# Kernel tuning notes

Hardware: AMD Instinct MI355X
Metric: run time of the kernel (lower is better)

## Reference

```python
import jax, jax.numpy as jnp
import numpy as np

NUM_USERS = 50000
NUM_ITEMS = 20000
N_NODES = NUM_USERS + NUM_ITEMS
D = 128
CONTENT_DIM = 512
BATCH = 8192
N_EDGES = 500000
NEG_SLOPE = 0.2  # GATConv leaky_relu slope


def setup_inputs() -> dict:
    key = jax.random.key(0)
    ks = jax.random.split(key, 16)
    return {
        "user_ids": jax.random.randint(ks[0], (BATCH,), 0, NUM_USERS),
        "item_ids": jax.random.randint(ks[1], (BATCH,), 0, NUM_ITEMS),
        "content_features": jax.random.normal(ks[2], (BATCH, CONTENT_DIM), jnp.float32),
        "edge_index": jax.random.randint(ks[3], (2, N_EDGES), 0, N_NODES),
        "user_emb_w": jax.random.normal(ks[4], (NUM_USERS, D), jnp.float32) * 0.05,
        "item_emb_w": jax.random.normal(ks[5], (NUM_ITEMS, D), jnp.float32) * 0.05,
        "content_proj_w": jax.random.normal(ks[6], (D, CONTENT_DIM), jnp.float32) * 0.04,
        "content_proj_b": jnp.zeros((D,), jnp.float32),
        "conv1_lin_w": jax.random.normal(ks[7], (2 * D, 2 * D), jnp.float32) * 0.06,
        "conv1_att_src": jax.random.normal(ks[8], (2, D), jnp.float32) * 0.1,
        "conv1_att_dst": jax.random.normal(ks[9], (2, D), jnp.float32) * 0.1,
        "conv1_bias": jnp.zeros((2 * D,), jnp.float32),
        "conv2_lin_w": jax.random.normal(ks[10], (D, 2 * D), jnp.float32) * 0.06,
        "conv2_att_src": jax.random.normal(ks[11], (1, D), jnp.float32) * 0.1,
        "conv2_att_dst": jax.random.normal(ks[12], (1, D), jnp.float32) * 0.1,
        "conv2_bias": jnp.zeros((D,), jnp.float32),
        "pred_w1": jax.random.normal(ks[13], (D, 3 * D), jnp.float32) * 0.05,
        "pred_b1": jnp.zeros((D,), jnp.float32),
        "pred_w2": jax.random.normal(ks[14], (1, D), jnp.float32) * 0.09,
        "pred_b2": jnp.zeros((1,), jnp.float32),
    }


def gat_conv(x, src, dst, lin_w, att_src, att_dst, bias, heads, out_ch):
    # PyG GATConv (shared lin for src/dst, concat=True, add_self_loops handled outside)
    n = x.shape[0]
    h = (x @ lin_w.T).reshape(n, heads, out_ch)          # [N,H,C]
    a_src = jnp.sum(h * att_src, axis=-1)                # [N,H]
    a_dst = jnp.sum(h * att_dst, axis=-1)                # [N,H]
    alpha = jax.nn.leaky_relu(a_src[src] + a_dst[dst], NEG_SLOPE)  # [E,H]
    # softmax over incoming edges of each destination node
    amax = jax.ops.segment_max(alpha, dst, num_segments=n)
    ex = jnp.exp(alpha - amax[dst])
    denom = jax.ops.segment_sum(ex, dst, num_segments=n)
    w = ex / denom[dst]                                  # [E,H]
    out = jax.ops.segment_sum(h[src] * w[:, :, None], dst, num_segments=n)
    return out.reshape(n, heads * out_ch) + bias


def _forward(user_ids, item_ids, edge_index, content_features, user_emb_w, item_emb_w,
             content_proj_w, content_proj_b, conv1_lin_w, conv1_att_src, conv1_att_dst,
             conv1_bias, conv2_lin_w, conv2_att_src, conv2_att_dst, conv2_bias,
             pred_w1, pred_b1, pred_w2, pred_b2):
    u_emb = user_emb_w[user_ids]                         # [B,D]
    i_emb = item_emb_w[item_ids]                         # [B,D]
    c_emb = content_features @ content_proj_w.T + content_proj_b  # [B,D]
    # scatter-init sparse node features (only batch nodes are nonzero, as in source)
    x = jnp.zeros((N_NODES, 2 * D), jnp.float32)
    x = x.at[user_ids].set(jnp.concatenate([u_emb, jnp.zeros_like(c_emb)], axis=1))
    x = x.at[NUM_USERS + item_ids].set(jnp.concatenate([i_emb, c_emb], axis=1))
    # add self loops (fill_value irrelevant: edge_weight unused by GATConv)
    loops = jnp.arange(N_NODES, dtype=edge_index.dtype)
    src = jnp.concatenate([edge_index[0], loops])
    dst = jnp.concatenate([edge_index[1], loops])
    x = jax.nn.elu(gat_conv(x, src, dst, conv1_lin_w, conv1_att_src, conv1_att_dst, conv1_bias, 2, D))
    # dropout inactive (eval mode)
    x = gat_conv(x, src, dst, conv2_lin_w, conv2_att_src, conv2_att_dst, conv2_bias, 1, D)
    combined = jnp.concatenate([u_emb, x[NUM_USERS + item_ids], x[user_ids]], axis=1)  # [B,3D]
    h = jax.nn.relu(combined @ pred_w1.T + pred_b1)
    return (h @ pred_w2.T + pred_b2).squeeze(-1)         # [B]


def reference(user_ids, item_ids, content_features, edge_index, user_emb_w, item_emb_w,
              content_proj_w, content_proj_b, conv1_lin_w, conv1_att_src, conv1_att_dst,
              conv1_bias, conv2_lin_w, conv2_att_src, conv2_att_dst, conv2_bias,
              pred_w1, pred_b1, pred_w2, pred_b2):
    return _forward(user_ids, item_ids, edge_index, content_features, user_emb_w, item_emb_w,
                    content_proj_w, content_proj_b, conv1_lin_w, conv1_att_src, conv1_att_dst,
                    conv1_bias, conv2_lin_w, conv2_att_src, conv2_att_dst, conv2_bias,
                    pred_w1, pred_b1, pred_w2, pred_b2)
```

## Files before the change

kernel.cpp:

```cpp
#include <hip/hip_runtime.h>
#include <hip/hip_bf16.h>

#define NU 50000
#define NI 20000
#define NN 70000
#define DD 128
#define BB 8192
#define EE 500000
#define ET 570000
#define NTASK 16384

__device__ __forceinline__ float lrelu(float x) { return x > 0.f ? x : 0.2f * x; }

typedef __attribute__((ext_vector_type(8))) short bf16x8;
typedef __attribute__((ext_vector_type(8))) unsigned short u16x8;
typedef __attribute__((ext_vector_type(4))) float f32x4;

__device__ __forceinline__ unsigned short f2bf_rne(float f) {
  unsigned int u = __builtin_bit_cast(unsigned int, f);
  u += 0x7FFFu + ((u >> 16) & 1u);
  return (unsigned short)(u >> 16);
}
__device__ __forceinline__ float bf2f(unsigned short h) {
  unsigned int u = ((unsigned int)h) << 16;
  return __builtin_bit_cast(float, u);
}

__global__ void split4_kernel(const float* __restrict__ w0, unsigned short* h0, unsigned short* l0, int n0,
                              const float* __restrict__ w1, unsigned short* h1, unsigned short* l1, int n1,
                              const float* __restrict__ w2, unsigned short* h2, unsigned short* l2, int n2,
                              const float* __restrict__ w3, unsigned short* h3, unsigned short* l3, int n3) {
  int i = blockIdx.x * 256 + threadIdx.x;
  const float* w; unsigned short* h; unsigned short* l; int idx;
  if (i < n0) { w = w0; h = h0; l = l0; idx = i; }
  else if (i < n0 + n1) { w = w1; h = h1; l = l1; idx = i - n0; }
  else if (i < n0 + n1 + n2) { w = w2; h = h2; l = l2; idx = i - n0 - n1; }
  else if (i < n0 + n1 + n2 + n3) { w = w3; h = h3; l = l3; idx = i - n0 - n1 - n2; }
  else return;
  float f = w[idx];
  unsigned short hh = f2bf_rne(f);
  h[idx] = hh;
  l[idx] = (unsigned short)(__builtin_bit_cast(unsigned int, f - bf2f(hh)) >> 16);
}

template <int GATHER>
__global__ __launch_bounds__(256) void gemm_mfma(
    const float* __restrict__ A,
    const unsigned short* __restrict__ Bh, const unsigned short* __restrict__ Bl,
    const float* __restrict__ bias, float* __restrict__ C,
    int M, int N, int K, int act,
    const int* __restrict__ uidx, const float* __restrict__ gA0,
    const float* __restrict__ gA1) {
  __shared__ __align__(16) unsigned short sAh[8][64][8];
  __shared__ __align__(16) unsigned short sAl[8][64][8];
  __shared__ __align__(16) unsigned short sBh[8][64][8];
  __shared__ __align__(16) unsigned short sBl[8][64][8];
  int tid = threadIdx.x;
  int bm = blockIdx.x * 64, bn = blockIdx.y * 64;
  int lane = tid & 63, w = tid >> 6;
  int wr = (w >> 1) * 32, wc = (w & 1) * 32;
  int fr = lane & 15, fk = lane >> 4;
  f32x4 acc[2][2] = {};

  for (int k0 = 0; k0 < K; k0 += 64) {
    __syncthreads();
#pragma unroll
    for (int t = 0; t < 2; t++) {
      int f = tid + t * 256;
      int row = f >> 3, kb = f & 7;
      int kg = k0 + kb * 8;
      const float* ap;
      if (GATHER) {
        int sec = kg >> 7;
        int kc = kg & 127;
        int r = bm + row;
        if (sec == 0)      ap = &gA0[(size_t)uidx[r] * 128 + kc];
        else if (sec == 1) ap = &gA1[((size_t)(BB + r)) * 128 + kc];
        else               ap = &gA1[((size_t)r) * 128 + kc];
      } else {
        ap = &A[(size_t)(bm + row) * K + kg];
      }
      float4 v0 = *reinterpret_cast<const float4*>(ap);
      float4 v1 = *reinterpret_cast<const float4*>(ap + 4);
      float vv[8] = {v0.x, v0.y, v0.z, v0.w, v1.x, v1.y, v1.z, v1.w};
      u16x8 hv, lv;
#pragma unroll
      for (int j = 0; j < 8; j++) {
        unsigned short hh = f2bf_rne(vv[j]);
        hv[j] = hh;
        lv[j] = (unsigned short)(__builtin_bit_cast(unsigned int, vv[j] - bf2f(hh)) >> 16);
      }
      *reinterpret_cast<u16x8*>(&sAh[kb][row][0]) = hv;
      *reinterpret_cast<u16x8*>(&sAl[kb][row][0]) = lv;
    }
#pragma unroll
    for (int t = 0; t < 2; t++) {
      int f = tid + t * 256;
      int row = f >> 3, kb = f & 7;
      int kg = k0 + kb * 8;
      *reinterpret_cast<u16x8*>(&sBh[kb][row][0]) =
          *reinterpret_cast<const u16x8*>(&Bh[(size_t)(bn + row) * K + kg]);
      *reinterpret_cast<u16x8*>(&sBl[kb][row][0]) =
          *reinterpret_cast<const u16x8*>(&Bl[(size_t)(bn + row) * K + kg]);
    }
    __syncthreads();
#pragma unroll
    for (int s = 0; s < 2; s++) {
      int kb = s * 4 + fk;
      bf16x8 ah0 = *reinterpret_cast<const bf16x8*>(&sAh[kb][wr + fr][0]);
      bf16x8 ah1 = *reinterpret_cast<const bf16x8*>(&sAh[kb][wr + 16 + fr][0]);
      bf16x8 al0 = *reinterpret_cast<const bf16x8*>(&sAl[kb][wr + fr][0]);
      bf16x8 al1 = *reinterpret_cast<const bf16x8*>(&sAl[kb][wr + 16 + fr][0]);
      bf16x8 bh0 = *reinterpret_cast<const bf16x8*>(&sBh[kb][wc + fr][0]);
      bf16x8 bh1 = *reinterpret_cast<const bf16x8*>(&sBh[kb][wc + 16 + fr][0]);
      bf16x8 bl0 = *reinterpret_cast<const bf16x8*>(&sBl[kb][wc + fr][0]);
      bf16x8 bl1 = *reinterpret_cast<const bf16x8*>(&sBl[kb][wc + 16 + fr][0]);
      acc[0][0] = __builtin_amdgcn_mfma_f32_16x16x32_bf16(al0, bh0, acc[0][0], 0, 0, 0);
      acc[0][0] = __builtin_amdgcn_mfma_f32_16x16x32_bf16(ah0, bl0, acc[0][0], 0, 0, 0);
      acc[0][0] = __builtin_amdgcn_mfma_f32_16x16x32_bf16(ah0, bh0, acc[0][0], 0, 0, 0);
      acc[0][1] = __builtin_amdgcn_mfma_f32_16x16x32_bf16(al0, bh1, acc[0][1], 0, 0, 0);
      acc[0][1] = __builtin_amdgcn_mfma_f32_16x16x32_bf16(ah0, bl1, acc[0][1], 0, 0, 0);
      acc[0][1] = __builtin_amdgcn_mfma_f32_16x16x32_bf16(ah0, bh1, acc[0][1], 0, 0, 0);
      acc[1][0] = __builtin_amdgcn_mfma_f32_16x16x32_bf16(al1, bh0, acc[1][0], 0, 0, 0);
      acc[1][0] = __builtin_amdgcn_mfma_f32_16x16x32_bf16(ah1, bl0, acc[1][0], 0, 0, 0);
      acc[1][0] = __builtin_amdgcn_mfma_f32_16x16x32_bf16(ah1, bh0, acc[1][0], 0, 0, 0);
      acc[1][1] = __builtin_amdgcn_mfma_f32_16x16x32_bf16(al1, bh1, acc[1][1], 0, 0, 0);
      acc[1][1] = __builtin_amdgcn_mfma_f32_16x16x32_bf16(ah1, bl1, acc[1][1], 0, 0, 0);
      acc[1][1] = __builtin_amdgcn_mfma_f32_16x16x32_bf16(ah1, bh1, acc[1][1], 0, 0, 0);
    }
  }
#pragma unroll
  for (int j = 0; j < 2; j++) {
    int col = bn + wc + j * 16 + fr;
    float bj = bias ? bias[col] : 0.f;
#pragma unroll
    for (int i = 0; i < 2; i++) {
#pragma unroll
      for (int r = 0; r < 4; r++) {
        int row = bm + wr + i * 16 + fk * 4 + r;
        float v = acc[i][j][r] + bj;
        if (act == 1) v = fmaxf(v, 0.f);
        C[(size_t)row * N + col] = v;
      }
    }
  }
}

__global__ void deg_winner_kernel(const int* __restrict__ ei, const int* __restrict__ iid,
                                  int* __restrict__ deg, int* __restrict__ winner) {
  int e = blockIdx.x * 256 + threadIdx.x;
  if (e < BB) atomicMax(&winner[iid[e]], e);
  if (e >= ET) return;
  int dst = (e < EE) ? ei[EE + e] : (e - EE);
  atomicAdd(&deg[dst], 1);
}

__global__ void build_xa_kernel(const int* __restrict__ uid, const int* __restrict__ iid,
                                const int* __restrict__ winner,
                                const float* __restrict__ uemb, const float* __restrict__ iemb,
                                const float* __restrict__ cemb,
                                float* __restrict__ Xa, int* __restrict__ map) {
  int t = blockIdx.x;
  int lane = threadIdx.x;
  int c4 = lane * 4;
  float4 v = make_float4(0.f, 0.f, 0.f, 0.f);
  int node;
  if (t < BB) {
    int u = uid[t];
    node = u;
    if (c4 < DD) v = *reinterpret_cast<const float4*>(&uemb[(size_t)u * DD + c4]);
  } else {
    int b = t - BB;
    int it = iid[b];
    node = NU + it;
    if (c4 < DD) {
      v = *reinterpret_cast<const float4*>(&iemb[(size_t)it * DD + c4]);
    } else {
      int wb = winner[it];
      v = *reinterpret_cast<const float4*>(&cemb[(size_t)wb * DD + (c4 - DD)]);
    }
  }
  *reinterpret_cast<float4*>(&Xa[(size_t)t * 256 + c4]) = v;
  if (lane == 0) map[node] = t;
}

__global__ void mark_kernel(const int* __restrict__ ei, const int* __restrict__ map,
                            unsigned char* __restrict__ needed) {
  int e = blockIdx.x * 256 + threadIdx.x;
  if (e >= ET) return;
  int src, dst;
  if (e < EE) { src = ei[e]; dst = ei[EE + e]; }
  else { src = e - EE; dst = src; }
  if (map[dst] >= 0) needed[src] = 1;
}

__global__ void rowstart_kernel(const int* __restrict__ deg, int* __restrict__ rowstart,
                                int* __restrict__ fill, int* __restrict__ counter) {
  int v = blockIdx.x * 256 + threadIdx.x;
  if (v >= NN) return;
  int s = atomicAdd(counter, deg[v]);
  rowstart[v] = s;
  fill[v] = s;
}

__global__ void fill_kernel(const int* __restrict__ ei, int* __restrict__ fill,
                            int* __restrict__ col) {
  int e = blockIdx.x * 256 + threadIdx.x;
  if (e >= ET) return;
  int src, dst;
  if (e < EE) { src = ei[e]; dst = ei[EE + e]; }
  else { src = e - EE; dst = src; }
  int pos = atomicAdd(&fill[dst], 1);
  col[pos] = src;
}

__global__ __launch_bounds__(256) void a1q_kernel(
    const int* __restrict__ uid, const int* __restrict__ iid,
    const float* __restrict__ Ha,
    const float* __restrict__ atts, const float* __restrict__ attd,
    const float* __restrict__ w2,
    const float* __restrict__ att2s, const float* __restrict__ att2d,
    float* __restrict__ a1s, float* __restrict__ a1d,
    float* __restrict__ qs, float* __restrict__ qd) {
  int t = blockIdx.x * 4 + (threadIdx.x >> 6);
  int lane = threadIdx.x & 63;
  if (t >= NTASK) {
    int k = (t - NTASK) * 64 + lane;
    float s = 0.f, d = 0.f;
#pragma unroll 4
    for (int j = 0; j < DD; j++) {
      float w = w2[(size_t)j * 256 + k];
      s += att2s[j] * w;
      d += att2d[j] * w;
    }
    qs[k] = s;
    qd[k] = d;
    return;
  }
  int v = (t < BB) ? uid[t] : NU + iid[t - BB];
  int head = lane >> 5, c = (lane & 31) * 4;
  float4 hv = *reinterpret_cast<const float4*>(&Ha[(size_t)t * 256 + head * DD + c]);
  float4 sv = *reinterpret_cast<const float4*>(&atts[head * DD + c]);
  float4 dv = *reinterpret_cast<const float4*>(&attd[head * DD + c]);
  float ps = hv.x * sv.x + hv.y * sv.y + hv.z * sv.z + hv.w * sv.w;
  float pd = hv.x * dv.x + hv.y * dv.y + hv.z * dv.z + hv.w * dv.w;
  for (int o = 1; o < 32; o <<= 1) { ps += __shfl_xor(ps, o); pd += __shfl_xor(pd, o); }
  if ((lane & 31) == 0) {
    a1s[(size_t)v * 2 + head] = ps;
    a1d[(size_t)v * 2 + head] = pd;
  }
}

__global__ __launch_bounds__(256) void conv1_agg_kernel(
    const int* __restrict__ col, const int* __restrict__ rowstart,
    const int* __restrict__ deg, const float* __restrict__ Ha,
    const int* __restrict__ map, const unsigned char* __restrict__ needed,
    const float* __restrict__ a1s, const float* __restrict__ a1d,
    const float* __restrict__ bias,
    const float* __restrict__ qs, const float* __restrict__ qd,
    unsigned short* __restrict__ x1b, float* __restrict__ a2s, float* __restrict__ a2d) {
  int v = blockIdx.x * 4 + (threadIdx.x >> 6);
  int lane = threadIdx.x & 63;
  if (!needed[v]) return;
  int head = lane >> 5;
  int d = deg[v], s0 = rowstart[v];
  float2 adv = *reinterpret_cast<const float2*>(&a1d[(size_t)v * 2]);
  float4 acc = make_float4(0.f, 0.f, 0.f, 0.f);
  float den;
  if (d <= 64) {
    bool act = lane < d;
    int ci = act ? col[s0 + lane] : 0;
    float2 asv = make_float2(0.f, 0.f);
    int ri = -1;
    if (act) {
      asv = *reinterpret_cast<const float2*>(&a1s[(size_t)ci * 2]);
      ri = map[ci];
    }
    float al0 = act ? lrelu(asv.x + adv.x) : -1e30f;
    float al1 = act ? lrelu(asv.y + adv.y) : -1e30f;
    float m0 = al0, m1 = al1;
#pragma unroll
    for (int o = 1; o < 64; o <<= 1) {
      m0 = fmaxf(m0, __shfl_xor(m0, o));
      m1 = fmaxf(m1, __shfl_xor(m1, o));
    }
    float ex0 = act ? __expf(al0 - m0) : 0.f;
    float ex1 = act ? __expf(al1 - m1) : 0.f;
    float cs0 = ex0, cs1 = ex1;
#pragma unroll
    for (int o = 1; o < 64; o <<= 1) {
      cs0 += __shfl_xor(cs0, o);
      cs1 += __shfl_xor(cs1, o);
    }
    den = head ? cs1 : cs0;
    for (int i2 = 0; i2 < d; i2++) {
      int r = __shfl(ri, i2);
      if (r >= 0) {
        float e0 = __shfl(ex0, i2), e1 = __shfl(ex1, i2);
        float ex = head ? e1 : e0;
        float4 hv = *reinterpret_cast<const float4*>(&Ha[((size_t)r << 8) + (lane << 2)]);
        acc.x += ex * hv.x; acc.y += ex * hv.y; acc.z += ex * hv.z; acc.w += ex * hv.w;
      }
    }
  } else {
    float m0 = -1e30f, m1 = -1e30f, den0 = 0.f, den1 = 0.f;
    for (int c0 = 0; c0 < d; c0 += 64) {
      int i = c0 + lane;
      bool act = i < d;
      int ci = act ? col[s0 + i] : 0;
      float2 asv = make_float2(0.f, 0.f);
      int ri = -1;
      if (act) {
        asv = *reinterpret_cast<const float2*>(&a1s[(size_t)ci * 2]);
        ri = map[ci];
      }
      float al0 = act ? lrelu(asv.x + adv.x) : -1e30f;
      float al1 = act ? lrelu(asv.y + adv.y) : -1e30f;
      float cm0 = al0, cm1 = al1;
#pragma unroll
      for (int o = 1; o < 64; o <<= 1) {
        cm0 = fmaxf(cm0, __shfl_xor(cm0, o));
        cm1 = fmaxf(cm1, __shfl_xor(cm1, o));
      }
      float nm0 = fmaxf(m0, cm0), nm1 = fmaxf(m1, cm1);
      float ex0 = act ? __expf(al0 - nm0) : 0.f;
      float ex1 = act ? __expf(al1 - nm1) : 0.f;
      float s0f = __expf(m0 - nm0), s1f = __expf(m1 - nm1);
      float cs0 = ex0, cs1 = ex1;
#pragma unroll
      for (int o = 1; o < 64; o <<= 1) {
        cs0 += __shfl_xor(cs0, o);
        cs1 += __shfl_xor(cs1, o);
      }
      den0 = den0 * s0f + cs0;
      den1 = den1 * s1f + cs1;
      float sc = head ? s1f : s0f;
      acc.x *= sc; acc.y *= sc; acc.z *= sc; acc.w *= sc;
      int n = min(64, d - c0);
      for (int i2 = 0; i2 < n; i2++) {
        int r = __shfl(ri, i2);
        if (r >= 0) {
          float e0 = __shfl(ex0, i2), e1 = __shfl(ex1, i2);
          float ex = head ? e1 : e0;
          float4 hv = *reinterpret_cast<const float4*>(&Ha[((size_t)r << 8) + (lane << 2)]);
          acc.x += ex * hv.x; acc.y += ex * hv.y; acc.z += ex * hv.z; acc.w += ex * hv.w;
        }
      }
      m0 = nm0; m1 = nm1;
    }
    den = head ? den1 : den0;
  }
  float inv = 1.f / den;
  float4 b4 = *reinterpret_cast<const float4*>(&bias[lane << 2]);
  float4 o;
  o.x = fmaf(acc.x, inv, b4.x);
  o.y = fmaf(acc.y, inv, b4.y);
  o.z = fmaf(acc.z, inv, b4.z);
  o.w = fmaf(acc.w, inv, b4.w);
  o.x = o.x > 0.f ? o.x : __expf(o.x) - 1.f;
  o.y = o.y > 0.f ? o.y : __expf(o.y) - 1.f;
  o.z = o.z > 0.f ? o.z : __expf(o.z) - 1.f;
  o.w = o.w > 0.f ? o.w : __expf(o.w) - 1.f;
  ushort4 st;
  st.x = f2bf_rne(o.x); st.y = f2bf_rne(o.y);
  st.z = f2bf_rne(o.z); st.w = f2bf_rne(o.w);
  *reinterpret_cast<ushort4*>(&x1b[((size_t)v << 8) + (lane << 2)]) = st;
  float4 sv = *reinterpret_cast<const float4*>(&qs[lane << 2]);
  float4 dv = *reinterpret_cast<const float4*>(&qd[lane << 2]);
  float ps = o.x * sv.x + o.y * sv.y + o.z * sv.z + o.w * sv.w;
  float pd = o.x * dv.x + o.y * dv.y + o.z * dv.z + o.w * dv.w;
#pragma unroll
  for (int of = 1; of < 64; of <<= 1) { ps += __shfl_xor(ps, of); pd += __shfl_xor(pd, of); }
  if (lane == 0) { a2s[v] = ps; a2d[v] = pd; }
}

__global__ __launch_bounds__(256) void conv2_agg_kernel(
    const int* __restrict__ uid, const int* __restrict__ iid,
    const int* __restrict__ col, const int* __restrict__ rowstart,
    const int* __restrict__ deg, const unsigned short* __restrict__ x1b,
    const float* __restrict__ a2s, const float* __restrict__ a2d,
    float* __restrict__ agg) {
  int t = blockIdx.x * 4 + (threadIdx.x >> 6);
  int lane = threadIdx.x & 63;
  int v = (t < BB) ? uid[t] : NU + iid[t - BB];
  int d = deg[v], s0 = rowstart[v];
  float ad = a2d[v];
  float4 acc = make_float4(0.f, 0.f, 0.f, 0.f);
  float den;
  if (d <= 64) {
    bool act = lane < d;
    int ci = act ? col[s0 + lane] : 0;
    float as = act ? a2s[ci] : 0.f;
    float al = act ? lrelu(as + ad) : -1e30f;
    float m = al;
#pragma unroll
    for (int o = 1; o < 64; o <<= 1) m = fmaxf(m, __shfl_xor(m, o));
    float ex = act ? __expf(al - m) : 0.f;
    float cs = ex;
#pragma unroll
    for (int o = 1; o < 64; o <<= 1) cs += __shfl_xor(cs, o);
    den = cs;
    for (int i2 = 0; i2 < d; i2++) {
      int r = __shfl(ci, i2);
      float e = __shfl(ex, i2);
      ushort4 hv = *reinterpret_cast<const ushort4*>(&x1b[((size_t)r << 8) + (lane << 2)]);
      acc.x += e * bf2f(hv.x); acc.y += e * bf2f(hv.y);
      acc.z += e * bf2f(hv.z); acc.w += e * bf2f(hv.w);
    }
  } else {
    float m = -1e30f; den = 0.f;
    for (int c0 = 0; c0 < d; c0 += 64) {
      int i = c0 + lane;
      bool act = i < d;
      int ci = act ? col[s0 + i] : 0;
      float as = act ? a2s[ci] : 0.f;
      float al = act ? lrelu(as + ad) : -1e30f;
      float cm = al;
#pragma unroll
      for (int o = 1; o < 64; o <<= 1) cm = fmaxf(cm, __shfl_xor(cm, o));
      float nm = fmaxf(m, cm);
      float ex = act ? __expf(al - nm) : 0.f;
      float sf = __expf(m - nm);
      float cs = ex;
#pragma unroll
      for (int o = 1; o < 64; o <<= 1) cs += __shfl_xor(cs, o);
      den = den * sf + cs;
      acc.x *= sf; acc.y *= sf; acc.z *= sf; acc.w *= sf;
      int n = min(64, d - c0);
      for (int i2 = 0; i2 < n; i2++) {
        int r = __shfl(ci, i2);
        float e = __shfl(ex, i2);
        ushort4 hv = *reinterpret_cast<const ushort4*>(&x1b[((size_t)r << 8) + (lane << 2)]);
        acc.x += e * bf2f(hv.x); acc.y += e * bf2f(hv.y);
        acc.z += e * bf2f(hv.z); acc.w += e * bf2f(hv.w);
      }
      m = nm;
    }
  }
  float inv = 1.f / den;
  float4 o = make_float4(acc.x * inv, acc.y * inv, acc.z * inv, acc.w * inv);
  *reinterpret_cast<float4*>(&agg[((size_t)t << 8) + (lane << 2)]) = o;
}

__global__ __launch_bounds__(256) void final_kernel(
    const float* __restrict__ ph, const float* __restrict__ w2,
    const float* __restrict__ b2, float* __restrict__ out) {
  int b = blockIdx.x * 4 + (threadIdx.x >> 6);
  int lane = threadIdx.x & 63;
  float2 hv = *reinterpret_cast<const float2*>(&ph[((size_t)b << 7) + (lane << 1)]);
  float2 wv = *reinterpret_cast<const float2*>(&w2[lane << 1]);
  float s = hv.x * wv.x + hv.y * wv.y;
  for (int o = 1; o < 64; o <<= 1) s += __shfl_xor(s, o);
  if (lane == 0) out[b] = s + b2[0];
}

extern "C" void kernel_launch(void* const* d_in, const int* in_sizes, int n_in,
                              void* d_out, int out_size, void* d_ws, size_t ws_size,
                              hipStream_t stream) {
  const int* uid = (const int*)d_in[0];
  const int* iid = (const int*)d_in[1];
  const float* content = (const float*)d_in[2];
  const int* ei = (const int*)d_in[3];
  const float* uemb = (const float*)d_in[4];
  const float* iemb = (const float*)d_in[5];
  const float* wc = (const float*)d_in[6];
  const float* bc = (const float*)d_in[7];
  const float* w1 = (const float*)d_in[8];
  const float* att1s = (const float*)d_in[9];
  const float* att1d = (const float*)d_in[10];
  const float* b1 = (const float*)d_in[11];
  const float* w2 = (const float*)d_in[12];
  const float* att2s = (const float*)d_in[13];
  const float* att2d = (const float*)d_in[14];
  const float* b2c = (const float*)d_in[15];
  const float* pw1 = (const float*)d_in[16];
  const float* pb1 = (const float*)d_in[17];
  const float* pw2 = (const float*)d_in[18];
  const float* pb2 = (const float*)d_in[19];
  float* out = (float*)d_out;
  char* ws = (char*)d_ws;

  size_t off = 0;
  auto alloc = [&](size_t bytes) {
    size_t o = off;
    off += (bytes + 255) & ~(size_t)255;
    return o;
  };
  size_t o_winner  = alloc(NI * 4);
  size_t o_map     = alloc(NN * 4);
  size_t o_a1s     = alloc((size_t)NN * 2 * 4);
  size_t o_a1d     = alloc((size_t)NN * 2 * 4);
  size_t o_deg     = alloc(NN * 4);
  size_t o_rs      = alloc(NN * 4);
  size_t o_fill    = alloc(NN * 4);
  size_t o_cnt     = alloc(4);
  size_t o_needed  = alloc(NN);
  size_t o_col     = alloc((size_t)ET * 4);
  size_t o_a2s     = alloc(NN * 4);
  size_t o_a2d     = alloc(NN * 4);
  size_t o_qs      = alloc(256 * 4);
  size_t o_qd      = alloc(256 * 4);
  size_t o_wch = alloc(65536 * 2),  o_wcl = alloc(65536 * 2);
  size_t o_w1h = alloc(65536 * 2),  o_w1l = alloc(65536 * 2);
  size_t o_w2h = alloc(32768 * 2),  o_w2l = alloc(32768 * 2);
  size_t o_p1h = alloc(49152 * 2),  o_p1l = alloc(49152 * 2);
  size_t o_r1      = alloc(4194304 + 16777216 + 16777216);
  size_t o_cemb  = o_r1;
  size_t o_xa    = o_r1 + 4194304;
  size_t o_ha    = o_r1 + 4194304 + 16777216;
  size_t o_agg   = o_r1;
  size_t o_out2c = o_r1 + 16777216;
  size_t o_ph    = o_r1;
  size_t o_x1b   = alloc((size_t)NN * 256 * 2);
  (void)ws_size; (void)in_sizes; (void)n_in; (void)out_size;

  int*   winner = (int*)(ws + o_winner);
  int*   map    = (int*)(ws + o_map);
  float* a1s    = (float*)(ws + o_a1s);
  float* a1d    = (float*)(ws + o_a1d);
  int*   deg    = (int*)(ws + o_deg);
  int*   rs     = (int*)(ws + o_rs);
  int*   fill   = (int*)(ws + o_fill);
  int*   cnt    = (int*)(ws + o_cnt);
  unsigned char* needed = (unsigned char*)(ws + o_needed);
  int*   col    = (int*)(ws + o_col);
  float* a2s    = (float*)(ws + o_a2s);
  float* a2d    = (float*)(ws + o_a2d);
  float* qs     = (float*)(ws + o_qs);
  float* qd     = (float*)(ws + o_qd);
  unsigned short* wch = (unsigned short*)(ws + o_wch);
  unsigned short* wcl = (unsigned short*)(ws + o_wcl);
  unsigned short* w1h = (unsigned short*)(ws + o_w1h);
  unsigned short* w1l = (unsigned short*)(ws + o_w1l);
  unsigned short* w2h = (unsigned short*)(ws + o_w2h);
  unsigned short* w2l = (unsigned short*)(ws + o_w2l);
  unsigned short* p1h = (unsigned short*)(ws + o_p1h);
  unsigned short* p1l = (unsigned short*)(ws + o_p1l);
  float* cemb   = (float*)(ws + o_cemb);
  float* Xa     = (float*)(ws + o_xa);
  float* Ha     = (float*)(ws + o_ha);
  float* agg    = (float*)(ws + o_agg);
  float* out2c  = (float*)(ws + o_out2c);
  float* ph     = (float*)(ws + o_ph);
  unsigned short* x1b = (unsigned short*)(ws + o_x1b);

  hipMemsetAsync(ws + o_winner, 0xFF, o_map - o_winner + (size_t)NN * 4, stream);
  hipMemsetAsync(ws + o_a1s, 0, o_a1d - o_a1s + (size_t)NN * 2 * 4, stream);
  hipMemsetAsync(ws + o_deg, 0, o_needed - o_deg + NN, stream);

  {
    int total = 65536 + 65536 + 32768 + 49152;
    split4_kernel<<<(total + 255) / 256, 256, 0, stream>>>(
        wc, wch, wcl, 65536, w1, w1h, w1l, 65536,
        w2, w2h, w2l, 32768, pw1, p1h, p1l, 49152);
  }
  deg_winner_kernel<<<(ET + 255) / 256, 256, 0, stream>>>(ei, iid, deg, winner);
  {
    dim3 g(BB / 64, DD / 64);
    gemm_mfma<0><<<g, 256, 0, stream>>>(content, wch, wcl, bc, cemb, BB, DD, 512, 0,
                                        nullptr, nullptr, nullptr);
  }
  build_xa_kernel<<<NTASK, 64, 0, stream>>>(uid, iid, winner, uemb, iemb, cemb, Xa, map);
  mark_kernel<<<(ET + 255) / 256, 256, 0, stream>>>(ei, map, needed);
  rowstart_kernel<<<(NN + 255) / 256, 256, 0, stream>>>(deg, rs, fill, cnt);
  fill_kernel<<<(ET + 255) / 256, 256, 0, stream>>>(ei, fill, col);
  {
    dim3 g(NTASK / 64, 256 / 64);
    gemm_mfma<0><<<g, 256, 0, stream>>>(Xa, w1h, w1l, nullptr, Ha, NTASK, 256, 256, 0,
                                        nullptr, nullptr, nullptr);
  }
  a1q_kernel<<<NTASK / 4 + 1, 256, 0, stream>>>(uid, iid, Ha, att1s, att1d,
                                                w2, att2s, att2d, a1s, a1d, qs, qd);
  conv1_agg_kernel<<<NN / 4, 256, 0, stream>>>(col, rs, deg, Ha, map, needed,
                                               a1s, a1d, b1, qs, qd, x1b, a2s, a2d);
  conv2_agg_kernel<<<NTASK / 4, 256, 0, stream>>>(uid, iid, col, rs, deg, x1b, a2s, a2d, agg);
  {
    dim3 g(NTASK / 64, DD / 64);
    gemm_mfma<0><<<g, 256, 0, stream>>>(agg, w2h, w2l, b2c, out2c, NTASK, DD, 256, 0,
                                        nullptr, nullptr, nullptr);
  }
  {
    dim3 g(BB / 64, DD / 64);
    gemm_mfma<1><<<g, 256, 0, stream>>>(nullptr, p1h, p1l, pb1, ph, BB, DD, 384, 1,
                                        uid, uemb, out2c);
  }
  final_kernel<<<BB / 4, 256, 0, stream>>>(ph, pw2, pb2, out);
}
```

Baseline: 230.5 us.

## Fuse setup kernels, gather content GEMM into Xa, dedupe conv2 tasks

Merges degree/winner counting, weight hi/lo splitting and Xa construction into one setup kernel, and folds mark into the CSR fill kernel. The content projection GEMM now computes only the winner rows and writes them straight into the Xa column slot through an index gather, removing the separate cemb buffer and copy. conv2 aggregation skips duplicate node tasks by checking map, and the predictor gathers through map. This cuts launches and redundant work but adds branching inside the merged kernels and indirect loads in the GEMMs.

```diff
diff --git a/kernel.cpp b/kernel.cpp
--- a/kernel.cpp
+++ b/kernel.cpp
@@ -26,31 +26,15 @@
   return __builtin_bit_cast(float, u);
 }
 
-__global__ void split4_kernel(const float* __restrict__ w0, unsigned short* h0, unsigned short* l0, int n0,
-                              const float* __restrict__ w1, unsigned short* h1, unsigned short* l1, int n1,
-                              const float* __restrict__ w2, unsigned short* h2, unsigned short* l2, int n2,
-                              const float* __restrict__ w3, unsigned short* h3, unsigned short* l3, int n3) {
-  int i = blockIdx.x * 256 + threadIdx.x;
-  const float* w; unsigned short* h; unsigned short* l; int idx;
-  if (i < n0) { w = w0; h = h0; l = l0; idx = i; }
-  else if (i < n0 + n1) { w = w1; h = h1; l = l1; idx = i - n0; }
-  else if (i < n0 + n1 + n2) { w = w2; h = h2; l = l2; idx = i - n0 - n1; }
-  else if (i < n0 + n1 + n2 + n3) { w = w3; h = h3; l = l3; idx = i - n0 - n1 - n2; }
-  else return;
-  float f = w[idx];
-  unsigned short hh = f2bf_rne(f);
-  h[idx] = hh;
-  l[idx] = (unsigned short)(__builtin_bit_cast(unsigned int, f - bf2f(hh)) >> 16);
-}
-
 template <int GATHER>
 __global__ __launch_bounds__(256) void gemm_mfma(
     const float* __restrict__ A,
     const unsigned short* __restrict__ Bh, const unsigned short* __restrict__ Bl,
-    const float* __restrict__ bias, float* __restrict__ C,
+    const float* __restrict__ bias, float* __restrict__ C, int ldc,
     int M, int N, int K, int act,
-    const int* __restrict__ uidx, const float* __restrict__ gA0,
-    const float* __restrict__ gA1) {
+    const int* __restrict__ idx0, const int* __restrict__ idx1,
+    const int* __restrict__ mapv,
+    const float* __restrict__ gA0, const float* __restrict__ gA1) {
   __shared__ __align__(16) unsigned short sAh[8][64][8];
   __shared__ __align__(16) unsigned short sAl[8][64][8];
   __shared__ __align__(16) unsigned short sBh[8][64][8];
@@ -70,13 +54,15 @@
       int row = f >> 3, kb = f & 7;
       int kg = k0 + kb * 8;
       const float* ap;
-      if (GATHER) {
+      if (GATHER == 1) {
         int sec = kg >> 7;
         int kc = kg & 127;
         int r = bm + row;
-        if (sec == 0)      ap = &gA0[(size_t)uidx[r] * 128 + kc];
-        else if (sec == 1) ap = &gA1[((size_t)(BB + r)) * 128 + kc];
-        else               ap = &gA1[((size_t)r) * 128 + kc];
+        if (sec == 0)      ap = &gA0[(size_t)idx0[r] * 128 + kc];
+        else if (sec == 1) ap = &gA1[(size_t)mapv[NU + idx1[r]] * 128 + kc];
+        else               ap = &gA1[(size_t)mapv[idx0[r]] * 128 + kc];
+      } else if (GATHER == 2) {
+        ap = &gA0[(size_t)idx0[bm + row] * K + kg];
       } else {
         ap = &A[(size_t)(bm + row) * K + kg];
       }
@@ -140,71 +126,80 @@
         int row = bm + wr + i * 16 + fk * 4 + r;
         float v = acc[i][j][r] + bj;
         if (act == 1) v = fmaxf(v, 0.f);
-        C[(size_t)row * N + col] = v;
-      }
-    }
-  }
-}
-
-__global__ void deg_winner_kernel(const int* __restrict__ ei, const int* __restrict__ iid,
-                                  int* __restrict__ deg, int* __restrict__ winner) {
-  int e = blockIdx.x * 256 + threadIdx.x;
-  if (e < BB) atomicMax(&winner[iid[e]], e);
-  if (e >= ET) return;
-  int dst = (e < EE) ? ei[EE + e] : (e - EE);
-  atomicAdd(&deg[dst], 1);
-}
-
-__global__ void build_xa_kernel(const int* __restrict__ uid, const int* __restrict__ iid,
-                                const int* __restrict__ winner,
-                                const float* __restrict__ uemb, const float* __restrict__ iemb,
-                                const float* __restrict__ cemb,
-                                float* __restrict__ Xa, int* __restrict__ map) {
-  int t = blockIdx.x;
-  int lane = threadIdx.x;
+        C[(size_t)row * ldc + col] = v;
+      }
+    }
+  }
+}
+
+#define EB 2227
+#define SPLB 832
+#define XAB 4096
+__global__ __launch_bounds__(256) void setup_kernel(
+    const int* __restrict__ ei, const int* __restrict__ uid, const int* __restrict__ iid,
+    int* __restrict__ deg, int* __restrict__ winner,
+    const float* __restrict__ wc, unsigned short* wch, unsigned short* wcl,
+    const float* __restrict__ w1, unsigned short* w1h, unsigned short* w1l,
+    const float* __restrict__ w2, unsigned short* w2h, unsigned short* w2l,
+    const float* __restrict__ pw1, unsigned short* p1h, unsigned short* p1l,
+    const float* __restrict__ uemb, const float* __restrict__ iemb,
+    float* __restrict__ Xa, int* __restrict__ map) {
+  int bid = blockIdx.x, tid = threadIdx.x;
+  if (bid < EB) {
+    int e = bid * 256 + tid;
+    if (e < BB) atomicMax(&winner[iid[e]], e);
+    if (e >= ET) return;
+    int dst = (e < EE) ? ei[EE + e] : (e - EE);
+    atomicAdd(&deg[dst], 1);
+    return;
+  }
+  if (bid < EB + SPLB) {
+    int i = (bid - EB) * 256 + tid;
+    const float* w; unsigned short* h; unsigned short* l; int idx;
+    if (i < 65536) { w = wc; h = wch; l = wcl; idx = i; }
+    else if (i < 131072) { w = w1; h = w1h; l = w1l; idx = i - 65536; }
+    else if (i < 163840) { w = w2; h = w2h; l = w2l; idx = i - 131072; }
+    else { w = pw1; h = p1h; l = p1l; idx = i - 163840; }
+    float f = w[idx];
+    unsigned short hh = f2bf_rne(f);
+    h[idx] = hh;
+    l[idx] = (unsigned short)(__builtin_bit_cast(unsigned int, f - bf2f(hh)) >> 16);
+    return;
+  }
+  int t = (bid - EB - SPLB) * 4 + (tid >> 6);
+  int lane = tid & 63;
   int c4 = lane * 4;
-  float4 v = make_float4(0.f, 0.f, 0.f, 0.f);
-  int node;
   if (t < BB) {
     int u = uid[t];
-    node = u;
+    float4 v = make_float4(0.f, 0.f, 0.f, 0.f);
     if (c4 < DD) v = *reinterpret_cast<const float4*>(&uemb[(size_t)u * DD + c4]);
+    *reinterpret_cast<float4*>(&Xa[(size_t)t * 256 + c4]) = v;
+    if (lane == 0) map[u] = t;
   } else {
-    int b = t - BB;
-    int it = iid[b];
-    node = NU + it;
+    int it = iid[t - BB];
     if (c4 < DD) {
-      v = *reinterpret_cast<const float4*>(&iemb[(size_t)it * DD + c4]);
-    } else {
-      int wb = winner[it];
-      v = *reinterpret_cast<const float4*>(&cemb[(size_t)wb * DD + (c4 - DD)]);
-    }
-  }
-  *reinterpret_cast<float4*>(&Xa[(size_t)t * 256 + c4]) = v;
-  if (lane == 0) map[node] = t;
-}
-
-__global__ void mark_kernel(const int* __restrict__ ei, const int* __restrict__ map,
-                            unsigned char* __restrict__ needed) {
-  int e = blockIdx.x * 256 + threadIdx.x;
-  if (e >= ET) return;
-  int src, dst;
-  if (e < EE) { src = ei[e]; dst = ei[EE + e]; }
-  else { src = e - EE; dst = src; }
-  if (map[dst] >= 0) needed[src] = 1;
-}
-
-__global__ void rowstart_kernel(const int* __restrict__ deg, int* __restrict__ rowstart,
-                                int* __restrict__ fill, int* __restrict__ counter) {
+      float4 v = *reinterpret_cast<const float4*>(&iemb[(size_t)it * DD + c4]);
+      *reinterpret_cast<float4*>(&Xa[(size_t)t * 256 + c4]) = v;
+    }
+    if (lane == 0) map[NU + it] = t;
+  }
+}
+
+__global__ void rowstart_kernel(const int* __restrict__ deg, const int* __restrict__ winner,
+                                const int* __restrict__ iid,
+                                int* __restrict__ rowstart, int* __restrict__ fill,
+                                int* __restrict__ counter, int* __restrict__ widx) {
   int v = blockIdx.x * 256 + threadIdx.x;
+  if (v < BB) widx[v] = winner[iid[v]];
   if (v >= NN) return;
   int s = atomicAdd(counter, deg[v]);
   rowstart[v] = s;
   fill[v] = s;
 }
 
-__global__ void fill_kernel(const int* __restrict__ ei, int* __restrict__ fill,
-                            int* __restrict__ col) {
+__global__ void fill_mark_kernel(const int* __restrict__ ei, int* __restrict__ fill,
+                                 int* __restrict__ col, const int* __restrict__ map,
+                                 unsigned char* __restrict__ needed) {
   int e = blockIdx.x * 256 + threadIdx.x;
   if (e >= ET) return;
   int src, dst;
@@ -212,6 +207,7 @@
   else { src = e - EE; dst = src; }
   int pos = atomicAdd(&fill[dst], 1);
   col[pos] = src;
+  if (map[dst] >= 0) needed[src] = 1;
 }
 
 __global__ __launch_bounds__(256) void a1q_kernel(
@@ -377,12 +373,14 @@
 __global__ __launch_bounds__(256) void conv2_agg_kernel(
     const int* __restrict__ uid, const int* __restrict__ iid,
     const int* __restrict__ col, const int* __restrict__ rowstart,
-    const int* __restrict__ deg, const unsigned short* __restrict__ x1b,
+    const int* __restrict__ deg, const int* __restrict__ map,
+    const unsigned short* __restrict__ x1b,
     const float* __restrict__ a2s, const float* __restrict__ a2d,
     float* __restrict__ agg) {
   int t = blockIdx.x * 4 + (threadIdx.x >> 6);
   int lane = threadIdx.x & 63;
   int v = (t < BB) ? uid[t] : NU + iid[t - BB];
+  if (map[v] != t) return;
   int d = deg[v], s0 = rowstart[v];
   float ad = a2d[v];
   float4 acc = make_float4(0.f, 0.f, 0.f, 0.f);
@@ -500,14 +498,14 @@
   size_t o_a2d     = alloc(NN * 4);
   size_t o_qs      = alloc(256 * 4);
   size_t o_qd      = alloc(256 * 4);
+  size_t o_widx    = alloc(BB * 4);
   size_t o_wch = alloc(65536 * 2),  o_wcl = alloc(65536 * 2);
   size_t o_w1h = alloc(65536 * 2),  o_w1l = alloc(65536 * 2);
   size_t o_w2h = alloc(32768 * 2),  o_w2l = alloc(32768 * 2);
   size_t o_p1h = alloc(49152 * 2),  o_p1l = alloc(49152 * 2);
-  size_t o_r1      = alloc(4194304 + 16777216 + 16777216);
-  size_t o_cemb  = o_r1;
-  size_t o_xa    = o_r1 + 4194304;
-  size_t o_ha    = o_r1 + 4194304 + 16777216;
+  size_t o_r1    = alloc(16777216 + 16777216);
+  size_t o_xa    = o_r1;
+  size_t o_ha    = o_r1 + 16777216;
   size_t o_agg   = o_r1;
   size_t o_out2c = o_r1 + 16777216;
   size_t o_ph    = o_r1;
@@ -528,6 +526,7 @@
   float* a2d    = (float*)(ws + o_a2d);
   float* qs     = (float*)(ws + o_qs);
   float* qd     = (float*)(ws + o_qd);
+  int*   widx   = (int*)(ws + o_widx);
   unsigned short* wch = (unsigned short*)(ws + o_wch);
   unsigned short* wcl = (unsigned short*)(ws + o_wcl);
   unsigned short* w1h = (unsigned short*)(ws + o_w1h);
@@ -536,7 +535,6 @@
   unsigned short* w2l = (unsigned short*)(ws + o_w2l);
   unsigned short* p1h = (unsigned short*)(ws + o_p1h);
   unsigned short* p1l = (unsigned short*)(ws + o_p1l);
-  float* cemb   = (float*)(ws + o_cemb);
   float* Xa     = (float*)(ws + o_xa);
   float* Ha     = (float*)(ws + o_ha);
   float* agg    = (float*)(ws + o_agg);
@@ -548,41 +546,38 @@
   hipMemsetAsync(ws + o_a1s, 0, o_a1d - o_a1s + (size_t)NN * 2 * 4, stream);
   hipMemsetAsync(ws + o_deg, 0, o_needed - o_deg + NN, stream);
 
-  {
-    int total = 65536 + 65536 + 32768 + 49152;
-    split4_kernel<<<(total + 255) / 256, 256, 0, stream>>>(
-        wc, wch, wcl, 65536, w1, w1h, w1l, 65536,
-        w2, w2h, w2l, 32768, pw1, p1h, p1l, 49152);
-  }
-  deg_winner_kernel<<<(ET + 255) / 256, 256, 0, stream>>>(ei, iid, deg, winner);
+  setup_kernel<<<EB + SPLB + XAB, 256, 0, stream>>>(
+      ei, uid, iid, deg, winner,
+      wc, wch, wcl, w1, w1h, w1l, w2, w2h, w2l, pw1, p1h, p1l,
+      uemb, iemb, Xa, map);
+  rowstart_kernel<<<(NN + 255) / 256, 256, 0, stream>>>(deg, winner, iid, rs, fill, cnt, widx);
   {
     dim3 g(BB / 64, DD / 64);
-    gemm_mfma<0><<<g, 256, 0, stream>>>(content, wch, wcl, bc, cemb, BB, DD, 512, 0,
-                                        nullptr, nullptr, nullptr);
-  }
-  build_xa_kernel<<<NTASK, 64, 0, stream>>>(uid, iid, winner, uemb, iemb, cemb, Xa, map);
-  mark_kernel<<<(ET + 255) / 256, 256, 0, stream>>>(ei, map, needed);
-  rowstart_kernel<<<(NN + 255) / 256, 256, 0, stream>>>(deg, rs, fill, cnt);
-  fill_kernel<<<(ET + 255) / 256, 256, 0, stream>>>(ei, fill, col);
+    gemm_mfma<2><<<g, 256, 0, stream>>>(nullptr, wch, wcl, bc, Xa + (size_t)BB * 256 + 128,
+                                        256, BB, DD, 512, 0,
+                                        widx, nullptr, nullptr, content, nullptr);
+  }
+  fill_mark_kernel<<<(ET + 255) / 256, 256, 0, stream>>>(ei, fill, col, map, needed);
   {
     dim3 g(NTASK / 64, 256 / 64);
-    gemm_mfma<0><<<g, 256, 0, stream>>>(Xa, w1h, w1l, nullptr, Ha, NTASK, 256, 256, 0,
-                                        nullptr, nullptr, nullptr);
+    gemm_mfma<0><<<g, 256, 0, stream>>>(Xa, w1h, w1l, nullptr, Ha, 256, NTASK, 256, 256, 0,
+                                        nullptr, nullptr, nullptr, nullptr, nullptr);
   }
   a1q_kernel<<<NTASK / 4 + 1, 256, 0, stream>>>(uid, iid, Ha, att1s, att1d,
                                                 w2, att2s, att2d, a1s, a1d, qs, qd);
   conv1_agg_kernel<<<NN / 4, 256, 0, stream>>>(col, rs, deg, Ha, map, needed,
                                                a1s, a1d, b1, qs, qd, x1b, a2s, a2d);
-  conv2_agg_kernel<<<NTASK / 4, 256, 0, stream>>>(uid, iid, col, rs, deg, x1b, a2s, a2d, agg);
+  conv2_agg_kernel<<<NTASK / 4, 256, 0, stream>>>(uid, iid, col, rs, deg, map,
+                                                  x1b, a2s, a2d, agg);
   {
     dim3 g(NTASK / 64, DD / 64);
-    gemm_mfma<0><<<g, 256, 0, stream>>>(agg, w2h, w2l, b2c, out2c, NTASK, DD, 256, 0,
-                                        nullptr, nullptr, nullptr);
+    gemm_mfma<0><<<g, 256, 0, stream>>>(agg, w2h, w2l, b2c, out2c, 128, NTASK, DD, 256, 0,
+                                        nullptr, nullptr, nullptr, nullptr, nullptr);
   }
   {
     dim3 g(BB / 64, DD / 64);
-    gemm_mfma<1><<<g, 256, 0, stream>>>(nullptr, p1h, p1l, pb1, ph, BB, DD, 384, 1,
-                                        uid, uemb, out2c);
+    gemm_mfma<1><<<g, 256, 0, stream>>>(nullptr, p1h, p1l, pb1, ph, 128, BB, DD, 384, 1,
+                                        uid, iid, map, uemb, out2c);
   }
   final_kernel<<<BB / 4, 256, 0, stream>>>(ph, pw2, pb2, out);
 }
```

Measured after the change: 224.2 us. 1.03x faster.
